# Performance work log

Measured on AMD Instinct MI355X. Metric: run time of the kernel, lower is better.

The kernel has to match this reference:

```python
import jax, jax.numpy as jnp
import numpy as np

B, S, D, E, K = 4, 4096, 2048, 64, 2

def setup_inputs() -> dict:
    key = jax.random.key(0)
    kx, kw = jax.random.split(key)
    x = jax.random.normal(kx, (B, S, D), dtype=jnp.float32)
    W = jax.random.normal(kw, (E, D), dtype=jnp.float32) * (1.0 / np.sqrt(D))
    b = jnp.zeros((E,), dtype=jnp.float32)
    return {"x": x, "W": W, "b": b, "k": K}

def reference(x, W, b, k):
    # logits: [B, S, E]
    logits = jnp.einsum('bsd,ed->bse', x, W) + b
    probs = jax.nn.softmax(logits, axis=-1)
    topk_probs, topk_experts = jax.lax.top_k(probs, k)  # [B,S,k]
    # one-hot over experts, OR-reduce over k -> bool mask [B,S,E]
    onehot = jax.nn.one_hot(topk_experts, E, dtype=jnp.int32)  # [B,S,k,E]
    masks = onehot.sum(axis=-2).astype(jnp.bool_)
    return (masks, probs)
```

## Files before the change

kernel.cpp:

```cpp
#include <hip/hip_runtime.h>
#include <math.h>

#define NTOK    16384
#define DDIM    2048
#define NEXP    64
#define PSTRIDE (NTOK * NEXP)
#define KP      512
#define PHASES  (DDIM / KP)
#define ROWP    (KP + 8)
#define HOFF    (NEXP * ROWP)

typedef _Float16 half8   __attribute__((ext_vector_type(8)));
typedef _Float16 half4   __attribute__((ext_vector_type(4)));
typedef float    floatx4 __attribute__((ext_vector_type(4)));

__global__ __launch_bounds__(256) void router_kernel(
    const float* __restrict__ x,
    const float* __restrict__ W,
    const float* __restrict__ bias,
    float* __restrict__ out)
{
    __shared__ _Float16 wlds[2 * NEXP * ROWP];

    const int tid  = threadIdx.x;
    const int lane = tid & 63;
    const int wid  = tid >> 6;
    const int t0   = blockIdx.x * 64;
    const int mrow = lane & 15;
    const int quad = lane >> 4;

    float bj[4];
#pragma unroll
    for (int j = 0; j < 4; ++j) bj[j] = bias[j * 16 + mrow];

    floatx4 acc_hh[4], acc_md[4];
#pragma unroll
    for (int j = 0; j < 4; ++j) { acc_hh[j] = (floatx4)0.0f; acc_md[j] = (floatx4)0.0f; }

    const float* xrow = x + (size_t)(t0 + wid * 16 + mrow) * DDIM + quad * 8;
    const _Float16* wh_frag = &wlds[mrow * ROWP + quad * 8];

    for (int p = 0; p < PHASES; ++p) {
        const int k0 = p * KP;

        __syncthreads();

#pragma unroll 8
        for (int i = 0; i < 32; ++i) {
            const int f  = tid + (i << 8);
            const int e  = f >> 7;
            const int kc = (f & 127) << 2;
            floatx4 w4 = *(const floatx4*)&W[(size_t)e * DDIM + k0 + kc];
            half4 h4, l4;
#pragma unroll
            for (int c = 0; c < 4; ++c) {
                float wv = w4[c];
                _Float16 h = (_Float16)wv;
                h4[c] = h;
                l4[c] = (_Float16)((wv - (float)h) * 2048.0f);
            }
            *((half4*)&wlds[e * ROWP + kc])        = h4;
            *((half4*)&wlds[HOFF + e * ROWP + kc]) = l4;
        }

        __syncthreads();

        const float* xp = xrow + k0;
#pragma unroll
        for (int s = 0; s < 16; ++s) {
            floatx4 v0 = *(const floatx4*)(xp + s * 32);
            floatx4 v1 = *(const floatx4*)(xp + s * 32 + 4);

            half8 a_hi, a_lo;
#pragma unroll
            for (int i = 0; i < 4; ++i) {
                float fv = v0[i];
                _Float16 h = (_Float16)fv;
                a_hi[i] = h;
                a_lo[i] = (_Float16)((fv - (float)h) * 2048.0f);
            }
#pragma unroll
            for (int i = 0; i < 4; ++i) {
                float fv = v1[i];
                _Float16 h = (_Float16)fv;
                a_hi[4 + i] = h;
                a_lo[4 + i] = (_Float16)((fv - (float)h) * 2048.0f);
            }

#pragma unroll
            for (int j = 0; j < 4; ++j) {
                const int ro = j * 16 * ROWP + s * 32;
                half8 bh = *(const half8*)(wh_frag + ro);
                half8 bl = *(const half8*)(wh_frag + HOFF + ro);
                acc_hh[j] = __builtin_amdgcn_mfma_f32_16x16x32_f16(a_hi, bh, acc_hh[j], 0, 0, 0);
                acc_md[j] = __builtin_amdgcn_mfma_f32_16x16x32_f16(a_hi, bl, acc_md[j], 0, 0, 0);
                acc_md[j] = __builtin_amdgcn_mfma_f32_16x16x32_f16(a_lo, bh, acc_md[j], 0, 0, 0);
            }
        }
    }

    const int c = mrow;
    float logit[4][4];
#pragma unroll
    for (int j = 0; j < 4; ++j)
#pragma unroll
        for (int r = 0; r < 4; ++r)
            logit[j][r] = acc_hh[j][r] + acc_md[j][r] * (1.0f / 2048.0f) + bj[j];

#pragma unroll
    for (int r = 0; r < 4; ++r) {
        const int trow = t0 + wid * 16 + quad * 4 + r;

        float m = logit[0][r];
#pragma unroll
        for (int j = 1; j < 4; ++j) m = fmaxf(m, logit[j][r]);
#pragma unroll
        for (int off = 1; off <= 8; off <<= 1) m = fmaxf(m, __shfl_xor(m, off));

        float pj[4], s = 0.0f;
#pragma unroll
        for (int j = 0; j < 4; ++j) { pj[j] = __expf(logit[j][r] - m); s += pj[j]; }
#pragma unroll
        for (int off = 1; off <= 8; off <<= 1) s += __shfl_xor(s, off);
        const float rinv = 1.0f / s;

        float v1 = -1e30f, v2 = -1e30f; int i1 = -1, i2 = -1;
#pragma unroll
        for (int j = 0; j < 4; ++j) {
            float v = logit[j][r]; int e = j * 16 + c;
            if (v > v1 || (v == v1 && e < i1)) { v2 = v1; i2 = i1; v1 = v; i1 = e; }
            else if (v > v2 || (v == v2 && e < i2)) { v2 = v; i2 = e; }
        }
#pragma unroll
        for (int off = 1; off <= 8; off <<= 1) {
            float u1 = __shfl_xor(v1, off); int q1 = __shfl_xor(i1, off);
            float u2 = __shfl_xor(v2, off); int q2 = __shfl_xor(i2, off);
            if (u1 > v1 || (u1 == v1 && q1 < i1)) {
                if (v1 > u2 || (v1 == u2 && i1 < q2)) { v2 = v1; i2 = i1; }
                else                                   { v2 = u2; i2 = q2; }
                v1 = u1; i1 = q1;
            } else {
                if (u1 > v2 || (u1 == v2 && q1 < i2)) { v2 = u1; i2 = q1; }
            }
        }

#pragma unroll
        for (int j = 0; j < 4; ++j) {
            const int col = j * 16 + c;
            const size_t o = (size_t)trow * NEXP + col;
            out[o]           = (col == i1 || col == i2) ? 1.0f : 0.0f;
            out[PSTRIDE + o] = pj[j] * rinv;
        }
    }
}

extern "C" void kernel_launch(void* const* d_in, const int* in_sizes, int n_in,
                              void* d_out, int out_size, void* d_ws, size_t ws_size,
                              hipStream_t stream) {
    const float* x = (const float*)d_in[0];
    const float* W = (const float*)d_in[1];
    const float* b = (const float*)d_in[2];
    (void)in_sizes; (void)n_in; (void)out_size; (void)d_ws; (void)ws_size;
    float* out = (float*)d_out;

    hipLaunchKernelGGL(router_kernel, dim3(NTOK / 64), dim3(256), 0, stream, x, W, b, out);
}
```

Before: 233.1 us.

## Split K across wave pairs with LDS reduction and halve phase size

```diff
diff --git a/kernel.cpp b/kernel.cpp
--- a/kernel.cpp
+++ b/kernel.cpp
@@ -5,7 +5,7 @@
 #define DDIM    2048
 #define NEXP    64
 #define PSTRIDE (NTOK * NEXP)
-#define KP      512
+#define KP      256
 #define PHASES  (DDIM / KP)
 #define ROWP    (KP + 8)
 #define HOFF    (NEXP * ROWP)
@@ -14,7 +14,7 @@
 typedef _Float16 half4   __attribute__((ext_vector_type(4)));
 typedef float    floatx4 __attribute__((ext_vector_type(4)));
 
-__global__ __launch_bounds__(256) void router_kernel(
+__global__ __launch_bounds__(256, 2) void router_kernel(
     const float* __restrict__ x,
     const float* __restrict__ W,
     const float* __restrict__ bias,
@@ -24,74 +24,76 @@
 
     const int tid  = threadIdx.x;
     const int lane = tid & 63;
-    const int wid  = tid >> 6;
-    const int t0   = blockIdx.x * 64;
+    const int wv   = tid >> 6;
+    const int t    = wv >> 1;
+    const int h    = wv & 1;
+    const int t0   = blockIdx.x * 32 + t * 16;
     const int mrow = lane & 15;
     const int quad = lane >> 4;
-
-    float bj[4];
-#pragma unroll
-    for (int j = 0; j < 4; ++j) bj[j] = bias[j * 16 + mrow];
 
     floatx4 acc_hh[4], acc_md[4];
 #pragma unroll
     for (int j = 0; j < 4; ++j) { acc_hh[j] = (floatx4)0.0f; acc_md[j] = (floatx4)0.0f; }
 
-    const float* xrow = x + (size_t)(t0 + wid * 16 + mrow) * DDIM + quad * 8;
-    const _Float16* wh_frag = &wlds[mrow * ROWP + quad * 8];
+    const float* xrow = x + (size_t)(t0 + mrow) * DDIM + h * 128 + quad * 8;
+    const _Float16* bfrag = &wlds[mrow * ROWP + h * 128 + quad * 8];
 
     for (int p = 0; p < PHASES; ++p) {
         const int k0 = p * KP;
 
         __syncthreads();
 
-#pragma unroll 8
-        for (int i = 0; i < 32; ++i) {
+#pragma unroll
+        for (int i = 0; i < 16; ++i) {
             const int f  = tid + (i << 8);
-            const int e  = f >> 7;
-            const int kc = (f & 127) << 2;
+            const int e  = f >> 6;
+            const int kc = (f & 63) << 2;
             floatx4 w4 = *(const floatx4*)&W[(size_t)e * DDIM + k0 + kc];
             half4 h4, l4;
 #pragma unroll
             for (int c = 0; c < 4; ++c) {
-                float wv = w4[c];
-                _Float16 h = (_Float16)wv;
-                h4[c] = h;
-                l4[c] = (_Float16)((wv - (float)h) * 2048.0f);
+                float wvv = w4[c];
+                _Float16 hh = (_Float16)wvv;
+                h4[c] = hh;
+                l4[c] = (_Float16)((wvv - (float)hh) * 2048.0f);
             }
             *((half4*)&wlds[e * ROWP + kc])        = h4;
             *((half4*)&wlds[HOFF + e * ROWP + kc]) = l4;
         }
 
+        const float* xp = xrow + k0;
+        floatx4 xv[8];
+#pragma unroll
+        for (int s = 0; s < 4; ++s) {
+            xv[2 * s]     = *(const floatx4*)(xp + s * 32);
+            xv[2 * s + 1] = *(const floatx4*)(xp + s * 32 + 4);
+        }
+
         __syncthreads();
 
-        const float* xp = xrow + k0;
 #pragma unroll
-        for (int s = 0; s < 16; ++s) {
-            floatx4 v0 = *(const floatx4*)(xp + s * 32);
-            floatx4 v1 = *(const floatx4*)(xp + s * 32 + 4);
-
+        for (int s = 0; s < 4; ++s) {
             half8 a_hi, a_lo;
 #pragma unroll
             for (int i = 0; i < 4; ++i) {
-                float fv = v0[i];
-                _Float16 h = (_Float16)fv;
-                a_hi[i] = h;
-                a_lo[i] = (_Float16)((fv - (float)h) * 2048.0f);
+                float fv = xv[2 * s][i];
+                _Float16 hh = (_Float16)fv;
+                a_hi[i] = hh;
+                a_lo[i] = (_Float16)((fv - (float)hh) * 2048.0f);
             }
 #pragma unroll
             for (int i = 0; i < 4; ++i) {
-                float fv = v1[i];
-                _Float16 h = (_Float16)fv;
-                a_hi[4 + i] = h;
-                a_lo[4 + i] = (_Float16)((fv - (float)h) * 2048.0f);
+                float fv = xv[2 * s + 1][i];
+                _Float16 hh = (_Float16)fv;
+                a_hi[4 + i] = hh;
+                a_lo[4 + i] = (_Float16)((fv - (float)hh) * 2048.0f);
             }
 
 #pragma unroll
             for (int j = 0; j < 4; ++j) {
                 const int ro = j * 16 * ROWP + s * 32;
-                half8 bh = *(const half8*)(wh_frag + ro);
-                half8 bl = *(const half8*)(wh_frag + HOFF + ro);
+                half8 bh = *(const half8*)(bfrag + ro);
+                half8 bl = *(const half8*)(bfrag + HOFF + ro);
                 acc_hh[j] = __builtin_amdgcn_mfma_f32_16x16x32_f16(a_hi, bh, acc_hh[j], 0, 0, 0);
                 acc_md[j] = __builtin_amdgcn_mfma_f32_16x16x32_f16(a_hi, bl, acc_md[j], 0, 0, 0);
                 acc_md[j] = __builtin_amdgcn_mfma_f32_16x16x32_f16(a_lo, bh, acc_md[j], 0, 0, 0);
@@ -99,17 +101,41 @@
         }
     }
 
+    __syncthreads();
+    float* rbuf = (float*)wlds;
+    if (h == 1) {
+#pragma unroll
+        for (int j = 0; j < 4; ++j)
+#pragma unroll
+            for (int r = 0; r < 4; ++r) {
+                rbuf[t * 2048 +        (j * 4 + r) * 64 + lane] = acc_hh[j][r];
+                rbuf[t * 2048 + 1024 + (j * 4 + r) * 64 + lane] = acc_md[j][r];
+            }
+    }
+    __syncthreads();
+    if (h == 1) return;
+
+#pragma unroll
+    for (int j = 0; j < 4; ++j)
+#pragma unroll
+        for (int r = 0; r < 4; ++r) {
+            acc_hh[j][r] += rbuf[t * 2048 +        (j * 4 + r) * 64 + lane];
+            acc_md[j][r] += rbuf[t * 2048 + 1024 + (j * 4 + r) * 64 + lane];
+        }
+
     const int c = mrow;
     float logit[4][4];
 #pragma unroll
-    for (int j = 0; j < 4; ++j)
+    for (int j = 0; j < 4; ++j) {
+        const float bj = bias[j * 16 + c];
 #pragma unroll
         for (int r = 0; r < 4; ++r)
-            logit[j][r] = acc_hh[j][r] + acc_md[j][r] * (1.0f / 2048.0f) + bj[j];
+            logit[j][r] = acc_hh[j][r] + acc_md[j][r] * (1.0f / 2048.0f) + bj;
+    }
 
 #pragma unroll
     for (int r = 0; r < 4; ++r) {
-        const int trow = t0 + wid * 16 + quad * 4 + r;
+        const int trow = t0 + quad * 4 + r;
 
         float m = logit[0][r];
 #pragma unroll
@@ -163,5 +189,5 @@
     (void)in_sizes; (void)n_in; (void)out_size; (void)d_ws; (void)ws_size;
     float* out = (float*)d_out;
 
-    hipLaunchKernelGGL(router_kernel, dim3(NTOK / 64), dim3(256), 0, stream, x, W, b, out);
+    hipLaunchKernelGGL(router_kernel, dim3(NTOK / 32), dim3(256), 0, stream, x, W, b, out);
 }
```

New measurement: 247.5 us. 1.06x slower.

## Precompute split-fp16 weights once and double-buffer LDS with register prefetch

Applied to the files above, without the earlier changes.

```diff
diff --git a/kernel.cpp b/kernel.cpp
--- a/kernel.cpp
+++ b/kernel.cpp
@@ -5,111 +5,149 @@
 #define DDIM    2048
 #define NEXP    64
 #define PSTRIDE (NTOK * NEXP)
-#define KP      512
-#define PHASES  (DDIM / KP)
-#define ROWP    (KP + 8)
-#define HOFF    (NEXP * ROWP)
+#define KP      256
+#define NPH     8
+#define ROWH    264
+#define PLANE   (NEXP * ROWH)
+#define SLICE   32768
 
 typedef _Float16 half8   __attribute__((ext_vector_type(8)));
 typedef _Float16 half4   __attribute__((ext_vector_type(4)));
 typedef float    floatx4 __attribute__((ext_vector_type(4)));
 
-__global__ __launch_bounds__(256) void router_kernel(
+__global__ __launch_bounds__(256) void wconv_kernel(
+    const float* __restrict__ W, _Float16* __restrict__ ws)
+{
+    const int idx4 = blockIdx.x * 256 + threadIdx.x;
+    const int e    = idx4 >> 9;
+    const int kg   = (idx4 & 511) << 2;
+    floatx4 w4 = *(const floatx4*)&W[(size_t)e * DDIM + kg];
+    half4 h4, l4;
+#pragma unroll
+    for (int c = 0; c < 4; ++c) {
+        float wv = w4[c];
+        _Float16 h = (_Float16)wv;
+        h4[c] = h;
+        l4[c] = (_Float16)((wv - (float)h) * 2048.0f);
+    }
+    const int p = kg >> 8, kl = kg & 255;
+    _Float16* dst = ws + (size_t)p * SLICE + e * 256 + kl;
+    *(half4*)dst           = h4;
+    *(half4*)(dst + 16384) = l4;
+}
+
+__global__ __launch_bounds__(256, 1) void router_kernel(
     const float* __restrict__ x,
-    const float* __restrict__ W,
+    const _Float16* __restrict__ ws,
     const float* __restrict__ bias,
     float* __restrict__ out)
 {
-    __shared__ _Float16 wlds[2 * NEXP * ROWP];
+    __shared__ _Float16 lds[2][2 * PLANE];
 
     const int tid  = threadIdx.x;
     const int lane = tid & 63;
     const int wid  = tid >> 6;
-    const int t0   = blockIdx.x * 64;
+    const int t0   = blockIdx.x * 64 + wid * 16;
     const int mrow = lane & 15;
     const int quad = lane >> 4;
 
-    float bj[4];
-#pragma unroll
-    for (int j = 0; j < 4; ++j) bj[j] = bias[j * 16 + mrow];
-
     floatx4 acc_hh[4], acc_md[4];
 #pragma unroll
     for (int j = 0; j < 4; ++j) { acc_hh[j] = (floatx4)0.0f; acc_md[j] = (floatx4)0.0f; }
 
-    const float* xrow = x + (size_t)(t0 + wid * 16 + mrow) * DDIM + quad * 8;
-    const _Float16* wh_frag = &wlds[mrow * ROWP + quad * 8];
-
-    for (int p = 0; p < PHASES; ++p) {
-        const int k0 = p * KP;
-
-        __syncthreads();
-
-#pragma unroll 8
-        for (int i = 0; i < 32; ++i) {
-            const int f  = tid + (i << 8);
-            const int e  = f >> 7;
-            const int kc = (f & 127) << 2;
-            floatx4 w4 = *(const floatx4*)&W[(size_t)e * DDIM + k0 + kc];
-            half4 h4, l4;
-#pragma unroll
-            for (int c = 0; c < 4; ++c) {
-                float wv = w4[c];
-                _Float16 h = (_Float16)wv;
-                h4[c] = h;
-                l4[c] = (_Float16)((wv - (float)h) * 2048.0f);
-            }
-            *((half4*)&wlds[e * ROWP + kc])        = h4;
-            *((half4*)&wlds[HOFF + e * ROWP + kc]) = l4;
-        }
-
-        __syncthreads();
-
-        const float* xp = xrow + k0;
-#pragma unroll
-        for (int s = 0; s < 16; ++s) {
-            floatx4 v0 = *(const floatx4*)(xp + s * 32);
-            floatx4 v1 = *(const floatx4*)(xp + s * 32 + 4);
-
+    const float* xrow = x + (size_t)(t0 + mrow) * DDIM + quad * 8;
+
+    floatx4 xc[16], xn[16];
+    half8   wn[16];
+
+#pragma unroll
+    for (int s = 0; s < 8; ++s) {
+        xc[2 * s]     = *(const floatx4*)(xrow + s * 32);
+        xc[2 * s + 1] = *(const floatx4*)(xrow + s * 32 + 4);
+    }
+#pragma unroll
+    for (int i = 0; i < 16; ++i)
+        wn[i] = *(const half8*)(ws + (size_t)(tid + i * 256) * 8);
+#pragma unroll
+    for (int i = 0; i < 16; ++i) {
+        const int c16 = tid + i * 256;
+        const int pl  = c16 >> 11, r = c16 & 2047;
+        *(half8*)&lds[0][pl * PLANE + (r >> 5) * ROWH + ((r & 31) << 3)] = wn[i];
+    }
+    __syncthreads();
+
+    const _Float16* lr = &lds[0][0];
+    _Float16*       lw = &lds[1][0];
+
+    for (int p = 0; p < NPH; ++p) {
+        if (p < NPH - 1) {
+            const float* xp = xrow + (p + 1) * KP;
+#pragma unroll
+            for (int s = 0; s < 8; ++s) {
+                xn[2 * s]     = *(const floatx4*)(xp + s * 32);
+                xn[2 * s + 1] = *(const floatx4*)(xp + s * 32 + 4);
+            }
+            const _Float16* wsrc = ws + (size_t)(p + 1) * SLICE;
+#pragma unroll
+            for (int i = 0; i < 16; ++i)
+                wn[i] = *(const half8*)(wsrc + (size_t)(tid + i * 256) * 8);
+        }
+
+#pragma unroll
+        for (int s = 0; s < 8; ++s) {
             half8 a_hi, a_lo;
 #pragma unroll
             for (int i = 0; i < 4; ++i) {
-                float fv = v0[i];
+                float fv = xc[2 * s][i];
                 _Float16 h = (_Float16)fv;
                 a_hi[i] = h;
                 a_lo[i] = (_Float16)((fv - (float)h) * 2048.0f);
             }
 #pragma unroll
             for (int i = 0; i < 4; ++i) {
-                float fv = v1[i];
+                float fv = xc[2 * s + 1][i];
                 _Float16 h = (_Float16)fv;
                 a_hi[4 + i] = h;
                 a_lo[4 + i] = (_Float16)((fv - (float)h) * 2048.0f);
             }
-
 #pragma unroll
             for (int j = 0; j < 4; ++j) {
-                const int ro = j * 16 * ROWP + s * 32;
-                half8 bh = *(const half8*)(wh_frag + ro);
-                half8 bl = *(const half8*)(wh_frag + HOFF + ro);
+                const _Float16* bb = lr + (j * 16 + mrow) * ROWH + s * 32 + quad * 8;
+                half8 bh = *(const half8*)bb;
+                half8 bl = *(const half8*)(bb + PLANE);
                 acc_hh[j] = __builtin_amdgcn_mfma_f32_16x16x32_f16(a_hi, bh, acc_hh[j], 0, 0, 0);
                 acc_md[j] = __builtin_amdgcn_mfma_f32_16x16x32_f16(a_hi, bl, acc_md[j], 0, 0, 0);
                 acc_md[j] = __builtin_amdgcn_mfma_f32_16x16x32_f16(a_lo, bh, acc_md[j], 0, 0, 0);
             }
         }
+
+        if (p < NPH - 1) {
+#pragma unroll
+            for (int i = 0; i < 16; ++i) {
+                const int c16 = tid + i * 256;
+                const int pl  = c16 >> 11, r = c16 & 2047;
+                *(half8*)&lw[pl * PLANE + (r >> 5) * ROWH + ((r & 31) << 3)] = wn[i];
+            }
+#pragma unroll
+            for (int i = 0; i < 16; ++i) xc[i] = xn[i];
+            _Float16* t = (_Float16*)lr; lr = lw; lw = t;
+        }
+        __syncthreads();
     }
 
     const int c = mrow;
     float logit[4][4];
 #pragma unroll
-    for (int j = 0; j < 4; ++j)
+    for (int j = 0; j < 4; ++j) {
+        const float bj = bias[j * 16 + c];
 #pragma unroll
         for (int r = 0; r < 4; ++r)
-            logit[j][r] = acc_hh[j][r] + acc_md[j][r] * (1.0f / 2048.0f) + bj[j];
+            logit[j][r] = acc_hh[j][r] + acc_md[j][r] * (1.0f / 2048.0f) + bj;
+    }
 
 #pragma unroll
     for (int r = 0; r < 4; ++r) {
-        const int trow = t0 + wid * 16 + quad * 4 + r;
+        const int trow = t0 + quad * 4 + r;
 
         float m = logit[0][r];
 #pragma unroll
@@ -160,8 +198,11 @@
     const float* x = (const float*)d_in[0];
     const float* W = (const float*)d_in[1];
     const float* b = (const float*)d_in[2];
-    (void)in_sizes; (void)n_in; (void)out_size; (void)d_ws; (void)ws_size;
+    (void)in_sizes; (void)n_in; (void)out_size; (void)ws_size;
     float* out = (float*)d_out;
 
-    hipLaunchKernelGGL(router_kernel, dim3(NTOK / 64), dim3(256), 0, stream, x, W, b, out);
+    _Float16* ws = (_Float16*)d_ws;
+
+    hipLaunchKernelGGL(wconv_kernel, dim3(128), dim3(256), 0, stream, W, ws);
+    hipLaunchKernelGGL(router_kernel, dim3(NTOK / 64), dim3(256), 0, stream, x, ws, b, out);
 }
```

Measured after the change: 215.6 us. 1.08x faster.
